# Performance work log

Measured on AMD Instinct MI355X. Metric: run time of the kernel, lower is better.

The kernel has to match this reference:

```python
import jax, jax.numpy as jnp
import numpy as np

N_USERS = 100000
N_ITEMS = 100000
N_EDGES = 200000
TBL = 50            # stored neighbor table width
D = 128             # node feature / embedding dim
TD = 128            # time encoding dim
E = D + TD          # attention embed dim (query = node||time)
H = 2               # heads
DH = E // H
NB = (20, 20)       # n_neighbors per layer
B = 2048
TMAX = 100000


def setup_inputs() -> dict:
    key = jax.random.key(0)
    ks = jax.random.split(key, 32)
    f32 = jnp.float32
    def nrm(k, sh, s):
        return jax.random.normal(k, sh, f32) * s
    inp = {}
    inp["nodes"] = jax.random.randint(ks[0], (B,), 0, N_USERS)
    inp["edges"] = jax.random.randint(ks[1], (B,), 0, N_EDGES)
    inp["timestamps"] = jax.random.randint(ks[2], (B,), 0, TMAX)
    inp["n_layers"] = 2
    # precomputed temporal neighbor tables (buffers) -- user neighbors are items & vice versa
    inp["user_neig"] = jax.random.randint(ks[3], (N_EDGES, TBL), 0, N_ITEMS)
    inp["user_edges"] = jax.random.randint(ks[4], (N_EDGES, TBL), 0, N_EDGES)
    inp["user_times"] = jax.random.randint(ks[5], (N_EDGES, TBL), 0, TMAX)
    inp["user_mask"] = jax.random.randint(ks[6], (N_EDGES, TBL), 0, 2)
    inp["item_neig"] = jax.random.randint(ks[7], (N_EDGES, TBL), 0, N_USERS)
    inp["item_edges"] = jax.random.randint(ks[8], (N_EDGES, TBL), 0, N_EDGES)
    inp["item_times"] = jax.random.randint(ks[9], (N_EDGES, TBL), 0, TMAX)
    inp["item_mask"] = jax.random.randint(ks[10], (N_EDGES, TBL), 0, 2)
    # learned params
    inp["user_emb"] = nrm(ks[11], (N_USERS, D), 0.1)
    inp["item_emb"] = nrm(ks[12], (N_ITEMS, D), 0.1)
    inp["time_w"] = jnp.asarray(1.0 / 10 ** np.linspace(0, 9, TD), f32)
    inp["time_b"] = jnp.zeros((TD,), f32)
    s = 1.0 / np.sqrt(E)
    L = 2
    inp["Wq"] = nrm(ks[13], (L, E, E), s); inp["bq"] = jnp.zeros((L, E), f32)
    inp["Wk"] = nrm(ks[14], (L, E, E), s); inp["bk"] = jnp.zeros((L, E), f32)
    inp["Wv"] = nrm(ks[15], (L, E, E), s); inp["bv"] = jnp.zeros((L, E), f32)
    inp["Wo"] = nrm(ks[16], (L, E, E), s); inp["bo"] = jnp.zeros((L, E), f32)
    inp["W1"] = nrm(ks[17], (L, D, E + D), 1.0 / np.sqrt(E + D)); inp["b1"] = jnp.zeros((L, D), f32)
    inp["W2"] = nrm(ks[18], (L, D, D), 1.0 / np.sqrt(D)); inp["b2"] = jnp.zeros((L, D), f32)
    return inp


def reference(nodes, edges, timestamps, n_layers,
              user_neig, user_edges, user_times, user_mask,
              item_neig, item_edges, item_times, item_mask,
              user_emb, item_emb, time_w, time_b,
              Wq, bq, Wk, bk, Wv, bv, Wo, bo, W1, b1, W2, b2):

    def tenc(t):  # TimeEncode: cos(t * w + b) -> [..., TD]
        return jnp.cos(t.astype(jnp.float32)[..., None] * time_w + time_b)

    def attend(l, node_feat, node_time, nbr_feat, edge_time, mask):
        # query: [N, E]; keys/values: [N, K, E]
        q = jnp.concatenate([node_feat, node_time], axis=-1)
        kv = jnp.concatenate([nbr_feat, edge_time], axis=-1)
        n, k = kv.shape[0], kv.shape[1]
        qh = (q @ Wq[l].T + bq[l]).reshape(n, H, DH)
        kh = (kv @ Wk[l].T + bk[l]).reshape(n, k, H, DH)
        vh = (kv @ Wv[l].T + bv[l]).reshape(n, k, H, DH)
        sc = jnp.einsum('nhd,nkhd->nhk', qh, kh) / np.sqrt(DH)
        valid = mask > 0  # [N, K]
        sc = jnp.where(valid[:, None, :], sc, -1e9)
        a = jax.nn.softmax(sc, axis=-1)
        o = jnp.einsum('nhk,nkhd->nhd', a, vh).reshape(n, E)
        o = o @ Wo[l].T + bo[l]
        o = jnp.where(valid.any(-1, keepdims=True), o, 0.0)  # zero all-invalid rows
        h = jax.nn.relu(jnp.concatenate([o, node_feat], axis=-1) @ W1[l].T + b1[l])
        return h @ W2[l].T + b2[l]

    def compute(nds, eds, tms, layer, is_user):
        nf = (user_emb if is_user else item_emb)[nds]
        if layer == 0:
            return nf
        k = NB[layer - 1]
        if is_user:
            neig, edg, tim, msk = user_neig, user_edges, user_times, user_mask
        else:
            neig, edg, tim, msk = item_neig, item_edges, item_times, item_mask
        adj = neig[eds][:, TBL - k:]   # [N, k] neighbor node ids (opposite type)
        ee = edg[eds][:, TBL - k:]
        tt = tim[eds][:, TBL - k:]
        mm = msk[eds][:, TBL - k:]
        deltas = tms[:, None] - tt
        nbr = compute(adj.reshape(-1), ee.reshape(-1), tt.reshape(-1), layer - 1, not is_user)
        nbr = nbr.reshape(nds.shape[0], k, -1)
        ntime = tenc(jnp.zeros_like(tms))
        etime = tenc(deltas)
        return attend(layer - 1, nf, ntime, nbr, etime, mm)

    return compute(nodes, edges, timestamps, int(n_layers), True)
```

## Files before the change

### kernel.cpp

```cpp
#include <hip/hip_runtime.h>
#include <hip/hip_bf16.h>

#define TBL 50
#define K 20
#define D 128
#define E 256
#define NB_B 2048
#define NSLOT (NB_B*K)
#define G 16

typedef unsigned short ushort;
typedef unsigned short ushort8 __attribute__((ext_vector_type(8)));
typedef float f32x4 __attribute__((ext_vector_type(4)));
typedef __bf16 bf16x8 __attribute__((ext_vector_type(8)));

#define OFF_GC    0
#define OFF_U     1024
#define OFF_CC    1536
#define OFF_PKF   2052
#define OFF_NBRB  264196
#define OFF_CNT   2885636
#define OFF_UEB   2926600
#define WS_NEED_F (OFF_UEB + 6400000)
#define APKo   0
#define VPKo   131072
#define OPKo   262144
#define W1PKo  393216
#define W2PKo  491520

__device__ __forceinline__ float cosr(float x) {
  const float HI = 0.15915493667125702f;
  const float LO = 6.4206383e-9f;
  float k = rintf(x * HI);
  float f = __fmaf_rn(x, HI, -k);
  f = __fmaf_rn(x, LO, f);
  return __builtin_amdgcn_cosf(f);
}
__device__ __forceinline__ float b2f(ushort u) {
  return __uint_as_float(((unsigned)u) << 16);
}
__device__ __forceinline__ ushort cvtbf(float f) {
  unsigned u = __float_as_uint(f);
  return (ushort)((u + 0x7FFF + ((u >> 16) & 1)) >> 16);
}
__device__ __forceinline__ bf16x8 ldb8(const ushort* p) {
  union { ushort8 u; bf16x8 b; } c;
  c.u = *(const ushort8*)p;
  return c.b;
}

__global__ __launch_bounds__(256) void precompute2(
    const float* __restrict__ Wq, const float* __restrict__ Wk,
    const float* __restrict__ bq, const float* __restrict__ bk,
    const float* __restrict__ time_b, float* __restrict__ ws)
{
  __shared__ float sqc[128], ctb[128];
  int b = blockIdx.x, t = threadIdx.x;
  ushort* wsu = (ushort*)(ws + OFF_PKF);
  if (b < 512) {
    int l = b >> 8, h = (b >> 7) & 1, i = b & 127;
    float s = 0.f;
    const float* wq = Wq + l*65536 + h*32768 + i;
    const float* wk = Wk + l*65536 + h*32768 + t;
    for (int m = 0; m < 128; m++) s += wq[m*256]*wk[m*256];
    int N = h*256 + t;
    int nt = N >> 4, cl = N & 15;
    int kk = i >> 5, ch = (i >> 3) & 3, bb = i & 7;
    wsu[APKo + (long)l*65536 + (((nt*4+kk)*64 + ch*16 + cl)*8) + bb] = cvtbf(s);
  } else {
    int q = b - 512, l = q >> 1, h = q & 1;
    if (t < 128) ctb[t] = cosf(time_b[t]);
    __syncthreads();
    if (t < 128) {
      int e = h*128 + t;
      float a = bq[l*256 + e];
      const float* wq = Wq + l*65536 + e*256 + 128;
      for (int m = 0; m < 128; m++) a += wq[m]*ctb[m];
      sqc[t] = a;
    }
    __syncthreads();
    { float s = 0.f;
      const float* wk = Wk + l*65536 + h*32768 + t;
      for (int m = 0; m < 128; m++) s += sqc[m]*wk[m*256];
      ws[OFF_GC + l*512 + h*256 + t] = s; }
    if (t < 128) {
      float s = 0.f;
      const float* wq = Wq + l*65536 + h*32768 + t;
      const float* bkp = bk + l*256 + h*128;
      for (int m = 0; m < 128; m++) s += wq[m*256]*bkp[m];
      ws[OFF_U + (l*2+h)*128 + t] = s; }
    if (t == 254) {
      float s = 0.f;
      const float* bkp = bk + l*256 + h*128;
      for (int m = 0; m < 128; m++) s += sqc[m]*bkp[m];
      ws[OFF_CC + l*2+h] = s; }
  }
}

__global__ __launch_bounds__(256) void packw(
    const float* __restrict__ Wv, const float* __restrict__ Wo,
    const float* __restrict__ W1, const float* __restrict__ W2,
    float* __restrict__ ws)
{
  int idx = blockIdx.x*256 + threadIdx.x;
  ushort* wsu = (ushort*)(ws + OFF_PKF);
  if (idx == 0) *(int*)(ws + OFF_CNT) = 0;
  if (idx < 131072) {
    int q = idx >> 15, r = idx & 32767, l = q >> 1, h = q & 1;
    int bb = r & 7, lane = (r >> 3) & 63, kk = (r >> 9) & 7, nt = r >> 12;
    int k = kk*32 + (lane>>4)*8 + bb, d = nt*16 + (lane&15);
    wsu[VPKo + idx] = cvtbf(Wv[l*65536 + (h*128+d)*256 + k]);
  } else if (idx < 262144) {
    int rel = idx - 131072, l = rel >> 16, r = rel & 65535;
    int bb = r & 7, lane = (r >> 3) & 63, kk = (r >> 9) & 7, nt = r >> 12;
    int k = kk*32 + (lane>>4)*8 + bb, e = nt*16 + (lane&15);
    wsu[OPKo + rel] = cvtbf(Wo[l*65536 + e*256 + k]);
  } else if (idx < 360448) {
    int rel = idx - 262144, l = rel / 49152, r = rel % 49152;
    int nt = r / 6144, rr = r - nt*6144;
    int kk = rr >> 9, lane = (rr >> 3) & 63, bb = rr & 7;
    int k = kk*32 + (lane>>4)*8 + bb, d = nt*16 + (lane&15);
    wsu[W1PKo + rel] = cvtbf(W1[l*49152 + d*384 + k]);
  } else {
    int rel = idx - 360448, l = rel >> 14, r = rel & 16383;
    int nt = r >> 11, rr = r & 2047;
    int kk = rr >> 9, lane = (rr >> 3) & 63, bb = rr & 7;
    int k = kk*32 + (lane>>4)*8 + bb, d = nt*16 + (lane&15);
    wsu[W2PKo + rel] = cvtbf(W2[l*16384 + d*128 + k]);
  }
}

__global__ __launch_bounds__(256) void pack_emb(
    const float* __restrict__ emb, float* __restrict__ ws)
{
  int idx = blockIdx.x*256 + threadIdx.x;
  if (idx < 1600000) {
    float4 a = ((const float4*)emb)[idx*2];
    float4 b = ((const float4*)emb)[idx*2+1];
    ushort8 o;
    o[0]=cvtbf(a.x); o[1]=cvtbf(a.y); o[2]=cvtbf(a.z); o[3]=cvtbf(a.w);
    o[4]=cvtbf(b.x); o[5]=cvtbf(b.y); o[6]=cvtbf(b.z); o[7]=cvtbf(b.w);
    ((ushort8*)(ws + OFF_UEB))[idx] = o;
  }
}

__global__ __launch_bounds__(256) void compact_valid(
    const int* __restrict__ edges, const int* __restrict__ u_mask,
    float* __restrict__ ws)
{
  int idx = blockIdx.x*256 + threadIdx.x;
  int b = idx / K, s = idx - b*K;
  int pe = edges[b];
  if (u_mask[pe*TBL + (TBL-K) + s] > 0) {
    int pos = atomicAdd((int*)(ws + OFF_CNT), 1);
    ((int*)(ws + OFF_CNT))[1 + pos] = idx;
  }
}

template<int LAYER, bool NBF16>
__global__ __launch_bounds__(256, 3) void attend(
    const int* __restrict__ nodes, const int* __restrict__ edges, const int* __restrict__ tstamps,
    const int* __restrict__ u_edges, const int* __restrict__ u_neig,
    const int* __restrict__ u_times, const int* __restrict__ u_mask,
    const int* __restrict__ i_neig, const int* __restrict__ i_times, const int* __restrict__ i_mask,
    const float* __restrict__ user_emb, const float* __restrict__ item_emb,
    const float* __restrict__ time_w, const float* __restrict__ time_b,
    const float* __restrict__ bv, const float* __restrict__ bo,
    const float* __restrict__ b1, const float* __restrict__ b2,
    float* __restrict__ wsf, float* __restrict__ out)
{
  __shared__ __align__(16) ushort sOP2[16*392];
  __shared__ __align__(16) ushort sGWS[16*520];
  __shared__ __align__(16) ushort sOP1[16*264];
  __shared__ float sTW[128], sTB[128], sAL[640], sQB[32];
  __shared__ int imem[96];
  __shared__ int nbm[960];

  const int tid = threadIdx.x, blk = blockIdx.x, l = LAYER;
  const int lane = tid & 63, wv = tid >> 6;
  const int col = lane & 15, chunk = lane >> 4;
  const ushort* wsu = (const ushort*)(wsf + OFF_PKF);
  const ushort* nbu = NBF16 ? ((LAYER == 0) ? (const ushort*)(wsf + OFF_UEB)
                                            : (const ushort*)(wsf + OFF_NBRB))
                            : (const ushort*)nullptr;
  const float*  nbf = user_emb;
  ushort* nbrOut = (ushort*)(wsf + OFF_NBRB);

  int count = (LAYER == 0) ? *(const int*)(wsf + OFF_CNT) : NB_B;
  if (blk*G >= count) return;

  if (tid < G) {
    int idx = blk*G + tid; int act = idx < count ? 1 : 0;
    int slot, nid, ntm, erow;
    if (LAYER == 0) {
      int ii = act ? idx : 0;
      slot = ((const int*)(wsf + OFF_CNT))[1 + ii];
      int bb = slot / K, s = slot - bb*K;
      int base = edges[bb]*TBL + (TBL-K) + s;
      nid = u_neig[base]; ntm = u_times[base]; erow = u_edges[base];
    } else { slot = idx; nid = nodes[idx]; ntm = tstamps[idx]; erow = edges[idx]; }
    imem[tid] = nid; imem[16+tid] = ntm; imem[32+tid] = erow;
    imem[48+tid] = slot; imem[80+tid] = act;
  }
  if (tid < 128) { sTW[tid] = time_w[tid]; sTB[tid] = time_b[tid]; }
  __syncthreads();

  const float* nemb = (LAYER == 0) ? item_emb : user_emb;
  #pragma unroll
  for (int it = 0; it < 8; it++) {
    int idx = tid + it*256, n = idx >> 7, i = idx & 127;
    sOP2[n*392 + 256 + i] = cvtbf(nemb[(long)imem[n]*D + i]);
  }
  #pragma unroll
  for (int it = 0; it < 2; it++) {
    int p = tid + it*256;
    if (p < G*K) {
      int n = p / K, k = p - n*K;
      int base = imem[32+n]*TBL + (TBL-K) + k;
      if (LAYER == 0) { nbm[p] = i_neig[base]; nbm[320+p] = i_times[base]; nbm[640+p] = i_mask[base]; }
      else            { nbm[p] = (blk*G+n)*K + k; nbm[320+p] = u_times[base]; nbm[640+p] = u_mask[base]; }
    }
  }
  __syncthreads();

  {
    bf16x8 a[4];
    #pragma unroll
    for (int kk = 0; kk < 4; kk++)
      a[kk] = ldb8(&sOP2[col*392 + 256 + kk*32 + chunk*8]);
    f32x4 acc[8];
    #pragma unroll
    for (int t = 0; t < 8; t++) acc[t] = (f32x4){0.f,0.f,0.f,0.f};
    const ushort* BP = wsu + APKo + (long)l*65536;
    #pragma unroll
    for (int t = 0; t < 8; t++) {
      int nt = wv*8 + t;
      #pragma unroll
      for (int kk = 0; kk < 4; kk++) {
        bf16x8 b = ldb8(&BP[((nt*4+kk)*64 + lane)*8]);
        acc[t] = __builtin_amdgcn_mfma_f32_16x16x32_bf16(a[kk], b, acc[t], 0, 0, 0);
      }
    }
    #pragma unroll
    for (int t = 0; t < 8; t++) {
      int N = (wv*8+t)*16 + col;
      float gcv = wsf[OFF_GC + l*512 + N];
      #pragma unroll
      for (int r = 0; r < 4; r++)
        sGWS[(chunk*4+r)*520 + N] = cvtbf(acc[t][r] + gcv);
    }
  }
  if (tid < 32) {
    int n = tid >> 1, h = tid & 1;
    float s = wsf[OFF_CC + l*2 + h];
    const float* u = wsf + OFF_U + (l*2+h)*128;
    for (int i = 0; i < 128; i++) s += b2f(sOP2[n*392 + 256 + i])*u[i];
    sQB[tid] = s;
  }
  __syncthreads();

  {
    auto scoreItem = [&](int p) {
      int n = p / K, k = p - n*K;
      float dtf = (float)(imem[16+n] - nbm[320+p]);
      const ushort8* gp = (const ushort8*)&sGWS[n*520];
      float a0 = 0.f, a1 = 0.f;
      if constexpr (NBF16) {
        const ushort8* fr8 = (const ushort8*)(nbu + (long)nbm[p]*D);
        #pragma unroll
        for (int half = 0; half < 2; half++) {
          ushort8 f[8];
          #pragma unroll
          for (int c = 0; c < 8; c++) f[c] = fr8[half*8 + c];
          #pragma unroll
          for (int c = 0; c < 8; c++) {
            ushort8 g0 = gp[half*8 + c], g1 = gp[32 + half*8 + c];
            float f0=b2f(f[c][0]),f1v=b2f(f[c][1]),f2=b2f(f[c][2]),f3=b2f(f[c][3]);
            float f4=b2f(f[c][4]),f5=b2f(f[c][5]),f6=b2f(f[c][6]),f7=b2f(f[c][7]);
            a0 += f0*b2f(g0[0]) + f1v*b2f(g0[1]) + f2*b2f(g0[2]) + f3*b2f(g0[3])
                + f4*b2f(g0[4]) + f5*b2f(g0[5]) + f6*b2f(g0[6]) + f7*b2f(g0[7]);
            a1 += f0*b2f(g1[0]) + f1v*b2f(g1[1]) + f2*b2f(g1[2]) + f3*b2f(g1[3])
                + f4*b2f(g1[4]) + f5*b2f(g1[5]) + f6*b2f(g1[6]) + f7*b2f(g1[7]);
          }
        }
      } else {
        const float4* fr = (const float4*)(nbf + (long)nbm[p]*D);
        #pragma unroll 4
        for (int c = 0; c < 16; c++) {
          float4 f0 = fr[2*c], f1 = fr[2*c+1];
          ushort8 g0 = gp[c], g1 = gp[32+c];
          a0 += f0.x*b2f(g0[0]) + f0.y*b2f(g0[1]) + f0.z*b2f(g0[2]) + f0.w*b2f(g0[3])
              + f1.x*b2f(g0[4]) + f1.y*b2f(g0[5]) + f1.z*b2f(g0[6]) + f1.w*b2f(g0[7]);
          a1 += f0.x*b2f(g1[0]) + f0.y*b2f(g1[1]) + f0.z*b2f(g1[2]) + f0.w*b2f(g1[3])
              + f1.x*b2f(g1[4]) + f1.y*b2f(g1[5]) + f1.z*b2f(g1[6]) + f1.w*b2f(g1[7]);
        }
      }
      #pragma unroll 2
      for (int c = 0; c < 16; c++) {
        ushort8 g0 = gp[16+c], g1 = gp[48+c];
        float a0c = 0.f, a1c = 0.f;
        #pragma unroll
        for (int j = 0; j < 8; j++) {
          float cv = cosr(__fadd_rn(__fmul_rn(dtf, sTW[c*8+j]), sTB[c*8+j]));
          a0c += cv*b2f(g0[j]); a1c += cv*b2f(g1[j]);
        }
        a0 += a0c; a1 += a1c;
      }
      int m = nbm[640+p];
      const float invsq = 0.08838834764831845f;
      sAL[n*40 + k]      = m > 0 ? (a0 + sQB[n*2])*invsq   : -1e9f;
      sAL[n*40 + 20 + k] = m > 0 ? (a1 + sQB[n*2+1])*invsq : -1e9f;
    };
    scoreItem(wv*80 + lane);
    if (lane < 16) scoreItem(wv*80 + 64 + lane);
  }
  __syncthreads();

  if (tid < 2*G) {
    int n = tid >> 1, h = tid & 1;
    float* a = &sAL[n*40 + h*20];
    float mx = -1e30f;
    for (int k = 0; k < K; k++) mx = fmaxf(mx, a[k]);
    float s = 0.f;
    for (int k = 0; k < K; k++) { float e = __expf(a[k]-mx); a[k] = e; s += e; }
    float inv = 1.f/s;
    for (int k = 0; k < K; k++) a[k] *= inv;
    if (h == 0) { int any = 0;
      for (int k = 0; k < K; k++) any |= nbm[640 + n*20 + k];
      imem[64+n] = any; }
  }
  __syncthreads();

  {
    const int n = tid >> 4, e0 = tid & 15;
    float w0[8], w1[8];
    #pragma unroll
    for (int i = 0; i < 8; i++) { w0[i] = 0.f; w1[i] = 0.f; }
    #pragma unroll 4
    for (int k = 0; k < K; k++) {
      float a0k = sAL[n*40 + k], a1k = sAL[n*40 + 20 + k];
      if constexpr (NBF16) {
        ushort8 f = *(const ushort8*)(nbu + (long)nbm[n*20+k]*D + e0*8);
        #pragma unroll
        for (int i = 0; i < 8; i++) {
          float fi = b2f(f[i]);
          w0[i] += a0k*fi; w1[i] += a1k*fi;
        }
      } else {
        const float* fr = nbf + (long)nbm[n*20+k]*D + e0*8;
        float4 fa = *(const float4*)fr, fb = *(const float4*)(fr+4);
        w0[0]+=a0k*fa.x; w1[0]+=a1k*fa.x; w0[1]+=a0k*fa.y; w1[1]+=a1k*fa.y;
        w0[2]+=a0k*fa.z; w1[2]+=a1k*fa.z; w0[3]+=a0k*fa.w; w1[3]+=a1k*fa.w;
        w0[4]+=a0k*fb.x; w1[4]+=a1k*fb.x; w0[5]+=a0k*fb.y; w1[5]+=a1k*fb.y;
        w0[6]+=a0k*fb.z; w1[6]+=a1k*fb.z; w0[7]+=a0k*fb.w; w1[7]+=a1k*fb.w;
      }
    }
    #pragma unroll
    for (int i = 0; i < 8; i++) {
      sGWS[n*520 + e0*8 + i]       = cvtbf(w0[i]);
      sGWS[n*520 + 256 + e0*8 + i] = cvtbf(w1[i]);
    }
    #pragma unroll
    for (int i = 0; i < 8; i++) { w0[i] = 0.f; w1[i] = 0.f; }
    float twv[8], tbv[8];
    #pragma unroll
    for (int i = 0; i < 8; i++) { twv[i] = sTW[e0*8+i]; tbv[i] = sTB[e0*8+i]; }
    for (int k = 0; k < K; k++) {
      float a0k = sAL[n*40 + k], a1k = sAL[n*40 + 20 + k];
      float dtf = (float)(imem[16+n] - nbm[320 + n*20 + k]);
      #pragma unroll
      for (int i = 0; i < 8; i++) {
        float c = cosr(__fadd_rn(__fmul_rn(dtf, twv[i]), tbv[i]));
        w0[i] += a0k*c; w1[i] += a1k*c;
      }
    }
    #pragma unroll
    for (int i = 0; i < 8; i++) {
      sGWS[n*520 + 128 + e0*8 + i] = cvtbf(w0[i]);
      sGWS[n*520 + 384 + e0*8 + i] = cvtbf(w1[i]);
    }
  }
  __syncthreads();

  {
    int h = wv >> 1, ntb = (wv & 1)*4;
    bf16x8 a[8];
    #pragma unroll
    for (int kk = 0; kk < 8; kk++)
      a[kk] = ldb8(&sGWS[col*520 + h*256 + kk*32 + chunk*8]);
    f32x4 acc[4];
    #pragma unroll
    for (int t = 0; t < 4; t++) acc[t] = (f32x4){0.f,0.f,0.f,0.f};
    const ushort* BP = wsu + VPKo + (long)(l*2+h)*32768;
    #pragma unroll
    for (int t = 0; t < 4; t++) {
      int nt = ntb + t;
      #pragma unroll
      for (int kk = 0; kk < 8; kk++) {
        bf16x8 b = ldb8(&BP[((nt*8+kk)*64 + lane)*8]);
        acc[t] = __builtin_amdgcn_mfma_f32_16x16x32_bf16(a[kk], b, acc[t], 0, 0, 0);
      }
    }
    #pragma unroll
    for (int t = 0; t < 4; t++) {
      int ocol = h*128 + (ntb+t)*16 + col;
      float bb = bv[l*256 + ocol];
      #pragma unroll
      for (int r = 0; r < 4; r++)
        sOP1[(chunk*4+r)*264 + ocol] = cvtbf(acc[t][r] + bb);
    }
  }
  __syncthreads();

  {
    bf16x8 a[8];
    #pragma unroll
    for (int kk = 0; kk < 8; kk++)
      a[kk] = ldb8(&sOP1[col*264 + kk*32 + chunk*8]);
    f32x4 acc[4];
    #pragma unroll
    for (int t = 0; t < 4; t++) acc[t] = (f32x4){0.f,0.f,0.f,0.f};
    const ushort* BP = wsu + OPKo + (long)l*65536;
    #pragma unroll
    for (int t = 0; t < 4; t++) {
      int nt = wv*4 + t;
      #pragma unroll
      for (int kk = 0; kk < 8; kk++) {
        bf16x8 b = ldb8(&BP[((nt*8+kk)*64 + lane)*8]);
        acc[t] = __builtin_amdgcn_mfma_f32_16x16x32_bf16(a[kk], b, acc[t], 0, 0, 0);
      }
    }
    #pragma unroll
    for (int t = 0; t < 4; t++) {
      int e = (wv*4+t)*16 + col;
      float bb = bo[l*256 + e];
      #pragma unroll
      for (int r = 0; r < 4; r++) {
        int row = chunk*4 + r;
        float v = imem[64+row] ? (acc[t][r] + bb) : 0.f;
        sOP2[row*392 + e] = cvtbf(v);
      }
    }
  }
  __syncthreads();

  {
    bf16x8 a[12];
    #pragma unroll
    for (int kk = 0; kk < 12; kk++)
      a[kk] = ldb8(&sOP2[col*392 + kk*32 + chunk*8]);
    f32x4 acc[2];
    acc[0] = (f32x4){0.f,0.f,0.f,0.f}; acc[1] = (f32x4){0.f,0.f,0.f,0.f};
    const ushort* BP = wsu + W1PKo + (long)l*49152;
    #pragma unroll
    for (int t = 0; t < 2; t++) {
      int nt = wv*2 + t;
      #pragma unroll
      for (int kk = 0; kk < 12; kk++) {
        bf16x8 b = ldb8(&BP[((nt*12+kk)*64 + lane)*8]);
        acc[t] = __builtin_amdgcn_mfma_f32_16x16x32_bf16(a[kk], b, acc[t], 0, 0, 0);
      }
    }
    #pragma unroll
    for (int t = 0; t < 2; t++) {
      int dcol = (wv*2+t)*16 + col;
      float bb = b1[l*128 + dcol];
      #pragma unroll
      for (int r = 0; r < 4; r++)
        sOP1[(chunk*4+r)*264 + dcol] = cvtbf(fmaxf(acc[t][r] + bb, 0.f));
    }
  }
  __syncthreads();

  {
    bf16x8 a[4];
    #pragma unroll
    for (int kk = 0; kk < 4; kk++)
      a[kk] = ldb8(&sOP1[col*264 + kk*32 + chunk*8]);
    f32x4 acc[2];
    acc[0] = (f32x4){0.f,0.f,0.f,0.f}; acc[1] = (f32x4){0.f,0.f,0.f,0.f};
    const ushort* BP = wsu + W2PKo + (long)l*16384;
    #pragma unroll
    for (int t = 0; t < 2; t++) {
      int nt = wv*2 + t;
      #pragma unroll
      for (int kk = 0; kk < 4; kk++) {
        bf16x8 b = ldb8(&BP[((nt*4+kk)*64 + lane)*8]);
        acc[t] = __builtin_amdgcn_mfma_f32_16x16x32_bf16(a[kk], b, acc[t], 0, 0, 0);
      }
    }
    #pragma unroll
    for (int t = 0; t < 2; t++) {
      int dcol = (wv*2+t)*16 + col;
      float bb = b2[l*128 + dcol];
      #pragma unroll
      for (int r = 0; r < 4; r++) {
        int row = chunk*4 + r;
        float v = acc[t][r] + bb;
        if (LAYER == 0) { if (imem[80+row]) nbrOut[(long)imem[48+row]*D + dcol] = cvtbf(v); }
        else            out[(long)(blk*G + row)*D + dcol] = v;
      }
    }
  }
}

extern "C" void kernel_launch(void* const* d_in, const int* in_sizes, int n_in,
                              void* d_out, int out_size, void* d_ws, size_t ws_size,
                              hipStream_t stream) {
  const int* nodes  = (const int*)d_in[0];
  const int* edges  = (const int*)d_in[1];
  const int* tst    = (const int*)d_in[2];
  const int* u_neig = (const int*)d_in[4];
  const int* u_edges= (const int*)d_in[5];
  const int* u_times= (const int*)d_in[6];
  const int* u_mask = (const int*)d_in[7];
  const int* i_neig = (const int*)d_in[8];
  const int* i_times= (const int*)d_in[10];
  const int* i_mask = (const int*)d_in[11];
  const float* user_emb = (const float*)d_in[12];
  const float* item_emb = (const float*)d_in[13];
  const float* time_w = (const float*)d_in[14];
  const float* time_b = (const float*)d_in[15];
  const float* Wq = (const float*)d_in[16]; const float* bq = (const float*)d_in[17];
  const float* Wk = (const float*)d_in[18]; const float* bk = (const float*)d_in[19];
  const float* Wv = (const float*)d_in[20]; const float* bv = (const float*)d_in[21];
  const float* Wo = (const float*)d_in[22]; const float* bo = (const float*)d_in[23];
  const float* W1 = (const float*)d_in[24]; const float* b1 = (const float*)d_in[25];
  const float* W2 = (const float*)d_in[26]; const float* b2 = (const float*)d_in[27];
  float* ws = (float*)d_ws;
  float* out = (float*)d_out;

  bool emb16 = ws_size >= (size_t)WS_NEED_F * 4;

  precompute2<<<dim3(516), dim3(256), 0, stream>>>(Wq, Wk, bq, bk, time_b, ws);
  packw<<<dim3(1536), dim3(256), 0, stream>>>(Wv, Wo, W1, W2, ws);
  if (emb16) pack_emb<<<dim3(6250), dim3(256), 0, stream>>>(user_emb, ws);
  compact_valid<<<dim3(160), dim3(256), 0, stream>>>(edges, u_mask, ws);

  if (emb16)
    attend<0,true><<<dim3(NSLOT/G), dim3(256), 0, stream>>>(
        nodes, edges, tst, u_edges, u_neig, u_times, u_mask,
        i_neig, i_times, i_mask, user_emb, item_emb, time_w, time_b,
        bv, bo, b1, b2, ws, out);
  else
    attend<0,false><<<dim3(NSLOT/G), dim3(256), 0, stream>>>(
        nodes, edges, tst, u_edges, u_neig, u_times, u_mask,
        i_neig, i_times, i_mask, user_emb, item_emb, time_w, time_b,
        bv, bo, b1, b2, ws, out);

  attend<1,true><<<dim3(NB_B/G), dim3(256), 0, stream>>>(
      nodes, edges, tst, u_edges, u_neig, u_times, u_mask,
      i_neig, i_times, i_mask, user_emb, item_emb, time_w, time_b,
      bv, bo, b1, b2, ws, out);
}
```

Before: 165.3 us.

## Switch bf16 storage and MFMA to fp16 with packed half2 score and aggregation math

Changes every packed weight, embedding and intermediate buffer from bf16 to fp16 and uses the f16 MFMA instead of the bf16 one. The score dot products and the attention-weighted aggregation now accumulate with packed __hfma2 in half precision rather than scalar fp32 FMAs. The score work is also rebalanced so all 256 threads take one full item, and the remaining 64 items are split four ways and combined with shuffles. This aims to halve the VALU work in the score and aggregation loops and to balance the lanes. The cost is fp16 overflow and accumulation-precision risk, notably in the half-precision accumulators and in the -1e9 mask values converted to half.

Result: faster. 143.3 us (-13.3%).

```diff
diff --git a/kernel.cpp b/kernel.cpp
--- a/kernel.cpp
+++ b/kernel.cpp
@@ -1,5 +1,6 @@
 #include <hip/hip_runtime.h>
 #include <hip/hip_bf16.h>
+#include <hip/hip_fp16.h>
 
 #define TBL 50
 #define K 20
@@ -12,7 +13,7 @@
 typedef unsigned short ushort;
 typedef unsigned short ushort8 __attribute__((ext_vector_type(8)));
 typedef float f32x4 __attribute__((ext_vector_type(4)));
-typedef __bf16 bf16x8 __attribute__((ext_vector_type(8)));
+typedef _Float16 half8 __attribute__((ext_vector_type(8)));
 
 #define OFF_GC    0
 #define OFF_U     1024
@@ -36,17 +37,16 @@
   f = __fmaf_rn(x, LO, f);
   return __builtin_amdgcn_cosf(f);
 }
-__device__ __forceinline__ float b2f(ushort u) {
-  return __uint_as_float(((unsigned)u) << 16);
-}
-__device__ __forceinline__ ushort cvtbf(float f) {
-  unsigned u = __float_as_uint(f);
-  return (ushort)((u + 0x7FFF + ((u >> 16) & 1)) >> 16);
-}
-__device__ __forceinline__ bf16x8 ldb8(const ushort* p) {
-  union { ushort8 u; bf16x8 b; } c;
+__device__ __forceinline__ ushort cvth(float f) {
+  union { _Float16 h; ushort u; } c; c.h = (_Float16)f; return c.u;
+}
+__device__ __forceinline__ float h2f(ushort u) {
+  union { ushort u; _Float16 h; } c; c.u = u; return (float)c.h;
+}
+__device__ __forceinline__ half8 ldh8(const ushort* p) {
+  union { ushort8 u; half8 h; } c;
   c.u = *(const ushort8*)p;
-  return c.b;
+  return c.h;
 }
 
 __global__ __launch_bounds__(256) void precompute2(
@@ -66,7 +66,7 @@
     int N = h*256 + t;
     int nt = N >> 4, cl = N & 15;
     int kk = i >> 5, ch = (i >> 3) & 3, bb = i & 7;
-    wsu[APKo + (long)l*65536 + (((nt*4+kk)*64 + ch*16 + cl)*8) + bb] = cvtbf(s);
+    wsu[APKo + (long)l*65536 + (((nt*4+kk)*64 + ch*16 + cl)*8) + bb] = cvth(s);
   } else {
     int q = b - 512, l = q >> 1, h = q & 1;
     if (t < 128) ctb[t] = cosf(time_b[t]);
@@ -109,24 +109,24 @@
     int q = idx >> 15, r = idx & 32767, l = q >> 1, h = q & 1;
     int bb = r & 7, lane = (r >> 3) & 63, kk = (r >> 9) & 7, nt = r >> 12;
     int k = kk*32 + (lane>>4)*8 + bb, d = nt*16 + (lane&15);
-    wsu[VPKo + idx] = cvtbf(Wv[l*65536 + (h*128+d)*256 + k]);
+    wsu[VPKo + idx] = cvth(Wv[l*65536 + (h*128+d)*256 + k]);
   } else if (idx < 262144) {
     int rel = idx - 131072, l = rel >> 16, r = rel & 65535;
     int bb = r & 7, lane = (r >> 3) & 63, kk = (r >> 9) & 7, nt = r >> 12;
     int k = kk*32 + (lane>>4)*8 + bb, e = nt*16 + (lane&15);
-    wsu[OPKo + rel] = cvtbf(Wo[l*65536 + e*256 + k]);
+    wsu[OPKo + rel] = cvth(Wo[l*65536 + e*256 + k]);
   } else if (idx < 360448) {
     int rel = idx - 262144, l = rel / 49152, r = rel % 49152;
     int nt = r / 6144, rr = r - nt*6144;
     int kk = rr >> 9, lane = (rr >> 3) & 63, bb = rr & 7;
     int k = kk*32 + (lane>>4)*8 + bb, d = nt*16 + (lane&15);
-    wsu[W1PKo + rel] = cvtbf(W1[l*49152 + d*384 + k]);
+    wsu[W1PKo + rel] = cvth(W1[l*49152 + d*384 + k]);
   } else {
     int rel = idx - 360448, l = rel >> 14, r = rel & 16383;
     int nt = r >> 11, rr = r & 2047;
     int kk = rr >> 9, lane = (rr >> 3) & 63, bb = rr & 7;
     int k = kk*32 + (lane>>4)*8 + bb, d = nt*16 + (lane&15);
-    wsu[W2PKo + rel] = cvtbf(W2[l*16384 + d*128 + k]);
+    wsu[W2PKo + rel] = cvth(W2[l*16384 + d*128 + k]);
   }
 }
 
@@ -138,8 +138,8 @@
     float4 a = ((const float4*)emb)[idx*2];
     float4 b = ((const float4*)emb)[idx*2+1];
     ushort8 o;
-    o[0]=cvtbf(a.x); o[1]=cvtbf(a.y); o[2]=cvtbf(a.z); o[3]=cvtbf(a.w);
-    o[4]=cvtbf(b.x); o[5]=cvtbf(b.y); o[6]=cvtbf(b.z); o[7]=cvtbf(b.w);
+    o[0]=cvth(a.x); o[1]=cvth(a.y); o[2]=cvth(a.z); o[3]=cvth(a.w);
+    o[4]=cvth(b.x); o[5]=cvth(b.y); o[6]=cvth(b.z); o[7]=cvth(b.w);
     ((ushort8*)(ws + OFF_UEB))[idx] = o;
   }
 }
@@ -209,7 +209,7 @@
   #pragma unroll
   for (int it = 0; it < 8; it++) {
     int idx = tid + it*256, n = idx >> 7, i = idx & 127;
-    sOP2[n*392 + 256 + i] = cvtbf(nemb[(long)imem[n]*D + i]);
+    sOP2[n*392 + 256 + i] = cvth(nemb[(long)imem[n]*D + i]);
   }
   #pragma unroll
   for (int it = 0; it < 2; it++) {
@@ -224,10 +224,10 @@
   __syncthreads();
 
   {
-    bf16x8 a[4];
+    half8 a[4];
     #pragma unroll
     for (int kk = 0; kk < 4; kk++)
-      a[kk] = ldb8(&sOP2[col*392 + 256 + kk*32 + chunk*8]);
+      a[kk] = ldh8(&sOP2[col*392 + 256 + kk*32 + chunk*8]);
     f32x4 acc[8];
     #pragma unroll
     for (int t = 0; t < 8; t++) acc[t] = (f32x4){0.f,0.f,0.f,0.f};
@@ -237,8 +237,8 @@
       int nt = wv*8 + t;
       #pragma unroll
       for (int kk = 0; kk < 4; kk++) {
-        bf16x8 b = ldb8(&BP[((nt*4+kk)*64 + lane)*8]);
-        acc[t] = __builtin_amdgcn_mfma_f32_16x16x32_bf16(a[kk], b, acc[t], 0, 0, 0);
+        half8 b = ldh8(&BP[((nt*4+kk)*64 + lane)*8]);
+        acc[t] = __builtin_amdgcn_mfma_f32_16x16x32_f16(a[kk], b, acc[t], 0, 0, 0);
       }
     }
     #pragma unroll
@@ -247,72 +247,94 @@
       float gcv = wsf[OFF_GC + l*512 + N];
       #pragma unroll
       for (int r = 0; r < 4; r++)
-        sGWS[(chunk*4+r)*520 + N] = cvtbf(acc[t][r] + gcv);
+        sGWS[(chunk*4+r)*520 + N] = cvth(acc[t][r] + gcv);
     }
   }
   if (tid < 32) {
     int n = tid >> 1, h = tid & 1;
     float s = wsf[OFF_CC + l*2 + h];
     const float* u = wsf + OFF_U + (l*2+h)*128;
-    for (int i = 0; i < 128; i++) s += b2f(sOP2[n*392 + 256 + i])*u[i];
+    for (int i = 0; i < 128; i++) s += h2f(sOP2[n*392 + 256 + i])*u[i];
     sQB[tid] = s;
   }
   __syncthreads();
 
   {
-    auto scoreItem = [&](int p) {
-      int n = p / K, k = p - n*K;
+    auto scorePart = [&](int p, int c0, int c1, float& r0, float& r1) {
+      int n = p / K;
       float dtf = (float)(imem[16+n] - nbm[320+p]);
-      const ushort8* gp = (const ushort8*)&sGWS[n*520];
-      float a0 = 0.f, a1 = 0.f;
+      const __half2* gp2 = (const __half2*)&sGWS[n*520];
+      __half2 z = __floats2half2_rn(0.f, 0.f);
+      __half2 A0 = z, B0 = z, A1 = z, B1 = z;
       if constexpr (NBF16) {
-        const ushort8* fr8 = (const ushort8*)(nbu + (long)nbm[p]*D);
-        #pragma unroll
-        for (int half = 0; half < 2; half++) {
-          ushort8 f[8];
-          #pragma unroll
-          for (int c = 0; c < 8; c++) f[c] = fr8[half*8 + c];
-          #pragma unroll
-          for (int c = 0; c < 8; c++) {
-            ushort8 g0 = gp[half*8 + c], g1 = gp[32 + half*8 + c];
-            float f0=b2f(f[c][0]),f1v=b2f(f[c][1]),f2=b2f(f[c][2]),f3=b2f(f[c][3]);
-            float f4=b2f(f[c][4]),f5=b2f(f[c][5]),f6=b2f(f[c][6]),f7=b2f(f[c][7]);
-            a0 += f0*b2f(g0[0]) + f1v*b2f(g0[1]) + f2*b2f(g0[2]) + f3*b2f(g0[3])
-                + f4*b2f(g0[4]) + f5*b2f(g0[5]) + f6*b2f(g0[6]) + f7*b2f(g0[7]);
-            a1 += f0*b2f(g1[0]) + f1v*b2f(g1[1]) + f2*b2f(g1[2]) + f3*b2f(g1[3])
-                + f4*b2f(g1[4]) + f5*b2f(g1[5]) + f6*b2f(g1[6]) + f7*b2f(g1[7]);
-          }
+        const __half2* fr2 = (const __half2*)(nbu + (long)nbm[p]*D);
+        for (int c = c0; c < c1; c++) {
+          __half2 f0 = fr2[c*4+0], f1 = fr2[c*4+1];
+          __half2 f2 = fr2[c*4+2], f3 = fr2[c*4+3];
+          A0 = __hfma2(f0, gp2[c*4+0], A0);     B0 = __hfma2(f1, gp2[c*4+1], B0);
+          A0 = __hfma2(f2, gp2[c*4+2], A0);     B0 = __hfma2(f3, gp2[c*4+3], B0);
+          A1 = __hfma2(f0, gp2[128+c*4+0], A1); B1 = __hfma2(f1, gp2[128+c*4+1], B1);
+          A1 = __hfma2(f2, gp2[128+c*4+2], A1); B1 = __hfma2(f3, gp2[128+c*4+3], B1);
         }
       } else {
-        const float4* fr = (const float4*)(nbf + (long)nbm[p]*D);
-        #pragma unroll 4
-        for (int c = 0; c < 16; c++) {
-          float4 f0 = fr[2*c], f1 = fr[2*c+1];
-          ushort8 g0 = gp[c], g1 = gp[32+c];
-          a0 += f0.x*b2f(g0[0]) + f0.y*b2f(g0[1]) + f0.z*b2f(g0[2]) + f0.w*b2f(g0[3])
-              + f1.x*b2f(g0[4]) + f1.y*b2f(g0[5]) + f1.z*b2f(g0[6]) + f1.w*b2f(g0[7]);
-          a1 += f0.x*b2f(g1[0]) + f0.y*b2f(g1[1]) + f0.z*b2f(g1[2]) + f0.w*b2f(g1[3])
-              + f1.x*b2f(g1[4]) + f1.y*b2f(g1[5]) + f1.z*b2f(g1[6]) + f1.w*b2f(g1[7]);
+        const float* fr = nbf + (long)nbm[p]*D;
+        for (int c = c0; c < c1; c++) {
+          __half2 f0 = __floats2half2_rn(fr[c*8+0], fr[c*8+1]);
+          __half2 f1 = __floats2half2_rn(fr[c*8+2], fr[c*8+3]);
+          __half2 f2 = __floats2half2_rn(fr[c*8+4], fr[c*8+5]);
+          __half2 f3 = __floats2half2_rn(fr[c*8+6], fr[c*8+7]);
+          A0 = __hfma2(f0, gp2[c*4+0], A0);     B0 = __hfma2(f1, gp2[c*4+1], B0);
+          A0 = __hfma2(f2, gp2[c*4+2], A0);     B0 = __hfma2(f3, gp2[c*4+3], B0);
+          A1 = __hfma2(f0, gp2[128+c*4+0], A1); B1 = __hfma2(f1, gp2[128+c*4+1], B1);
+          A1 = __hfma2(f2, gp2[128+c*4+2], A1); B1 = __hfma2(f3, gp2[128+c*4+3], B1);
         }
       }
-      #pragma unroll 2
-      for (int c = 0; c < 16; c++) {
-        ushort8 g0 = gp[16+c], g1 = gp[48+c];
-        float a0c = 0.f, a1c = 0.f;
-        #pragma unroll
-        for (int j = 0; j < 8; j++) {
-          float cv = cosr(__fadd_rn(__fmul_rn(dtf, sTW[c*8+j]), sTB[c*8+j]));
-          a0c += cv*b2f(g0[j]); a1c += cv*b2f(g1[j]);
-        }
-        a0 += a0c; a1 += a1c;
-      }
+      for (int c = c0; c < c1; c++) {
+        int j = c*8;
+        __half2 cA = __floats2half2_rn(
+            cosr(__fadd_rn(__fmul_rn(dtf, sTW[j+0]), sTB[j+0])),
+            cosr(__fadd_rn(__fmul_rn(dtf, sTW[j+1]), sTB[j+1])));
+        __half2 cB = __floats2half2_rn(
+            cosr(__fadd_rn(__fmul_rn(dtf, sTW[j+2]), sTB[j+2])),
+            cosr(__fadd_rn(__fmul_rn(dtf, sTW[j+3]), sTB[j+3])));
+        __half2 cC = __floats2half2_rn(
+            cosr(__fadd_rn(__fmul_rn(dtf, sTW[j+4]), sTB[j+4])),
+            cosr(__fadd_rn(__fmul_rn(dtf, sTW[j+5]), sTB[j+5])));
+        __half2 cD = __floats2half2_rn(
+            cosr(__fadd_rn(__fmul_rn(dtf, sTW[j+6]), sTB[j+6])),
+            cosr(__fadd_rn(__fmul_rn(dtf, sTW[j+7]), sTB[j+7])));
+        A0 = __hfma2(cA, gp2[64+c*4+0], A0);     B0 = __hfma2(cB, gp2[64+c*4+1], B0);
+        A0 = __hfma2(cC, gp2[64+c*4+2], A0);     B0 = __hfma2(cD, gp2[64+c*4+3], B0);
+        A1 = __hfma2(cA, gp2[192+c*4+0], A1);    B1 = __hfma2(cB, gp2[192+c*4+1], B1);
+        A1 = __hfma2(cC, gp2[192+c*4+2], A1);    B1 = __hfma2(cD, gp2[192+c*4+3], B1);
+      }
+      __half2 S0 = __hadd2(A0, B0), S1 = __hadd2(A1, B1);
+      r0 = __low2float(S0) + __high2float(S0);
+      r1 = __low2float(S1) + __high2float(S1);
+    };
+    const float invsq = 0.08838834764831845f;
+    {
+      int p = tid;
+      float a0, a1;
+      scorePart(p, 0, 16, a0, a1);
+      int n = p / K, k = p - n*K;
       int m = nbm[640+p];
-      const float invsq = 0.08838834764831845f;
       sAL[n*40 + k]      = m > 0 ? (a0 + sQB[n*2])*invsq   : -1e9f;
       sAL[n*40 + 20 + k] = m > 0 ? (a1 + sQB[n*2+1])*invsq : -1e9f;
-    };
-    scoreItem(wv*80 + lane);
-    if (lane < 16) scoreItem(wv*80 + 64 + lane);
+    }
+    {
+      int p = 256 + (tid >> 2), sub = tid & 3;
+      float a0, a1;
+      scorePart(p, sub*4, sub*4+4, a0, a1);
+      a0 += __shfl_xor(a0, 1); a0 += __shfl_xor(a0, 2);
+      a1 += __shfl_xor(a1, 1); a1 += __shfl_xor(a1, 2);
+      if (sub == 0) {
+        int n = p / K, k = p - n*K;
+        int m = nbm[640+p];
+        sAL[n*40 + k]      = m > 0 ? (a0 + sQB[n*2])*invsq   : -1e9f;
+        sAL[n*40 + 20 + k] = m > 0 ? (a1 + sQB[n*2+1])*invsq : -1e9f;
+      }
+    }
   }
   __syncthreads();
 
@@ -333,61 +355,69 @@
 
   {
     const int n = tid >> 4, e0 = tid & 15;
-    float w0[8], w1[8];
-    #pragma unroll
-    for (int i = 0; i < 8; i++) { w0[i] = 0.f; w1[i] = 0.f; }
+    __half2 z = __floats2half2_rn(0.f, 0.f);
+    __half2 W0[4], W1[4];
+    #pragma unroll
+    for (int i = 0; i < 4; i++) { W0[i] = z; W1[i] = z; }
     #pragma unroll 4
     for (int k = 0; k < K; k++) {
-      float a0k = sAL[n*40 + k], a1k = sAL[n*40 + 20 + k];
+      __half2 a0h = __half2half2(__float2half(sAL[n*40 + k]));
+      __half2 a1h = __half2half2(__float2half(sAL[n*40 + 20 + k]));
       if constexpr (NBF16) {
-        ushort8 f = *(const ushort8*)(nbu + (long)nbm[n*20+k]*D + e0*8);
+        const __half2* f2 = (const __half2*)(nbu + (long)nbm[n*20+k]*D + e0*8);
         #pragma unroll
-        for (int i = 0; i < 8; i++) {
-          float fi = b2f(f[i]);
-          w0[i] += a0k*fi; w1[i] += a1k*fi;
+        for (int i = 0; i < 4; i++) {
+          __half2 f = f2[i];
+          W0[i] = __hfma2(a0h, f, W0[i]);
+          W1[i] = __hfma2(a1h, f, W1[i]);
         }
       } else {
         const float* fr = nbf + (long)nbm[n*20+k]*D + e0*8;
-        float4 fa = *(const float4*)fr, fb = *(const float4*)(fr+4);
-        w0[0]+=a0k*fa.x; w1[0]+=a1k*fa.x; w0[1]+=a0k*fa.y; w1[1]+=a1k*fa.y;
-        w0[2]+=a0k*fa.z; w1[2]+=a1k*fa.z; w0[3]+=a0k*fa.w; w1[3]+=a1k*fa.w;
-        w0[4]+=a0k*fb.x; w1[4]+=a1k*fb.x; w0[5]+=a0k*fb.y; w1[5]+=a1k*fb.y;
-        w0[6]+=a0k*fb.z; w1[6]+=a1k*fb.z; w0[7]+=a0k*fb.w; w1[7]+=a1k*fb.w;
-      }
-    }
-    #pragma unroll
-    for (int i = 0; i < 8; i++) {
-      sGWS[n*520 + e0*8 + i]       = cvtbf(w0[i]);
-      sGWS[n*520 + 256 + e0*8 + i] = cvtbf(w1[i]);
-    }
-    #pragma unroll
-    for (int i = 0; i < 8; i++) { w0[i] = 0.f; w1[i] = 0.f; }
+        #pragma unroll
+        for (int i = 0; i < 4; i++) {
+          __half2 f = __floats2half2_rn(fr[2*i], fr[2*i+1]);
+          W0[i] = __hfma2(a0h, f, W0[i]);
+          W1[i] = __hfma2(a1h, f, W1[i]);
+        }
+      }
+    }
+    #pragma unroll
+    for (int i = 0; i < 4; i++) {
+      *(__half2*)&sGWS[n*520 + e0*8 + 2*i]       = W0[i];
+      *(__half2*)&sGWS[n*520 + 256 + e0*8 + 2*i] = W1[i];
+    }
+    #pragma unroll
+    for (int i = 0; i < 4; i++) { W0[i] = z; W1[i] = z; }
     float twv[8], tbv[8];
     #pragma unroll
     for (int i = 0; i < 8; i++) { twv[i] = sTW[e0*8+i]; tbv[i] = sTB[e0*8+i]; }
     for (int k = 0; k < K; k++) {
-      float a0k = sAL[n*40 + k], a1k = sAL[n*40 + 20 + k];
+      __half2 a0h = __half2half2(__float2half(sAL[n*40 + k]));
+      __half2 a1h = __half2half2(__float2half(sAL[n*40 + 20 + k]));
       float dtf = (float)(imem[16+n] - nbm[320 + n*20 + k]);
       #pragma unroll
-      for (int i = 0; i < 8; i++) {
-        float c = cosr(__fadd_rn(__fmul_rn(dtf, twv[i]), tbv[i]));
-        w0[i] += a0k*c; w1[i] += a1k*c;
-      }
-    }
-    #pragma unroll
-    for (int i = 0; i < 8; i++) {
-      sGWS[n*520 + 128 + e0*8 + i] = cvtbf(w0[i]);
-      sGWS[n*520 + 384 + e0*8 + i] = cvtbf(w1[i]);
+      for (int i = 0; i < 4; i++) {
+        __half2 c2 = __floats2half2_rn(
+            cosr(__fadd_rn(__fmul_rn(dtf, twv[2*i]),   tbv[2*i])),
+            cosr(__fadd_rn(__fmul_rn(dtf, twv[2*i+1]), tbv[2*i+1])));
+        W0[i] = __hfma2(a0h, c2, W0[i]);
+        W1[i] = __hfma2(a1h, c2, W1[i]);
+      }
+    }
+    #pragma unroll
+    for (int i = 0; i < 4; i++) {
+      *(__half2*)&sGWS[n*520 + 128 + e0*8 + 2*i] = W0[i];
+      *(__half2*)&sGWS[n*520 + 384 + e0*8 + 2*i] = W1[i];
     }
   }
   __syncthreads();
 
   {
     int h = wv >> 1, ntb = (wv & 1)*4;
-    bf16x8 a[8];
+    half8 a[8];
     #pragma unroll
     for (int kk = 0; kk < 8; kk++)
-      a[kk] = ldb8(&sGWS[col*520 + h*256 + kk*32 + chunk*8]);
+      a[kk] = ldh8(&sGWS[col*520 + h*256 + kk*32 + chunk*8]);
     f32x4 acc[4];
     #pragma unroll
     for (int t = 0; t < 4; t++) acc[t] = (f32x4){0.f,0.f,0.f,0.f};
@@ -397,8 +427,8 @@
       int nt = ntb + t;
       #pragma unroll
       for (int kk = 0; kk < 8; kk++) {
-        bf16x8 b = ldb8(&BP[((nt*8+kk)*64 + lane)*8]);
-        acc[t] = __builtin_amdgcn_mfma_f32_16x16x32_bf16(a[kk], b, acc[t], 0, 0, 0);
+        half8 b = ldh8(&BP[((nt*8+kk)*64 + lane)*8]);
+        acc[t] = __builtin_amdgcn_mfma_f32_16x16x32_f16(a[kk], b, acc[t], 0, 0, 0);
       }
     }
     #pragma unroll
@@ -407,16 +437,16 @@
       float bb = bv[l*256 + ocol];
       #pragma unroll
       for (int r = 0; r < 4; r++)
-        sOP1[(chunk*4+r)*264 + ocol] = cvtbf(acc[t][r] + bb);
-    }
-  }
-  __syncthreads();
-
-  {
-    bf16x8 a[8];
+        sOP1[(chunk*4+r)*264 + ocol] = cvth(acc[t][r] + bb);
+    }
+  }
+  __syncthreads();
+
+  {
+    half8 a[8];
     #pragma unroll
     for (int kk = 0; kk < 8; kk++)
-      a[kk] = ldb8(&sOP1[col*264 + kk*32 + chunk*8]);
+      a[kk] = ldh8(&sOP1[col*264 + kk*32 + chunk*8]);
     f32x4 acc[4];
     #pragma unroll
     for (int t = 0; t < 4; t++) acc[t] = (f32x4){0.f,0.f,0.f,0.f};
@@ -426,8 +456,8 @@
       int nt = wv*4 + t;
       #pragma unroll
       for (int kk = 0; kk < 8; kk++) {
-        bf16x8 b = ldb8(&BP[((nt*8+kk)*64 + lane)*8]);
-        acc[t] = __builtin_amdgcn_mfma_f32_16x16x32_bf16(a[kk], b, acc[t], 0, 0, 0);
+        half8 b = ldh8(&BP[((nt*8+kk)*64 + lane)*8]);
+        acc[t] = __builtin_amdgcn_mfma_f32_16x16x32_f16(a[kk], b, acc[t], 0, 0, 0);
       }
     }
     #pragma unroll
@@ -438,17 +468,17 @@
       for (int r = 0; r < 4; r++) {
         int row = chunk*4 + r;
         float v = imem[64+row] ? (acc[t][r] + bb) : 0.f;
-        sOP2[row*392 + e] = cvtbf(v);
-      }
-    }
-  }
-  __syncthreads();
-
-  {
-    bf16x8 a[12];
+        sOP2[row*392 + e] = cvth(v);
+      }
+    }
+  }
+  __syncthreads();
+
+  {
+    half8 a[12];
     #pragma unroll
     for (int kk = 0; kk < 12; kk++)
-      a[kk] = ldb8(&sOP2[col*392 + kk*32 + chunk*8]);
+      a[kk] = ldh8(&sOP2[col*392 + kk*32 + chunk*8]);
     f32x4 acc[2];
     acc[0] = (f32x4){0.f,0.f,0.f,0.f}; acc[1] = (f32x4){0.f,0.f,0.f,0.f};
     const ushort* BP = wsu + W1PKo + (long)l*49152;
@@ -457,8 +487,8 @@
       int nt = wv*2 + t;
       #pragma unroll
       for (int kk = 0; kk < 12; kk++) {
-        bf16x8 b = ldb8(&BP[((nt*12+kk)*64 + lane)*8]);
-        acc[t] = __builtin_amdgcn_mfma_f32_16x16x32_bf16(a[kk], b, acc[t], 0, 0, 0);
+        half8 b = ldh8(&BP[((nt*12+kk)*64 + lane)*8]);
+        acc[t] = __builtin_amdgcn_mfma_f32_16x16x32_f16(a[kk], b, acc[t], 0, 0, 0);
       }
     }
     #pragma unroll
@@ -467,16 +497,16 @@
       float bb = b1[l*128 + dcol];
       #pragma unroll
       for (int r = 0; r < 4; r++)
-        sOP1[(chunk*4+r)*264 + dcol] = cvtbf(fmaxf(acc[t][r] + bb, 0.f));
-    }
-  }
-  __syncthreads();
-
-  {
-    bf16x8 a[4];
+        sOP1[(chunk*4+r)*264 + dcol] = cvth(fmaxf(acc[t][r] + bb, 0.f));
+    }
+  }
+  __syncthreads();
+
+  {
+    half8 a[4];
     #pragma unroll
     for (int kk = 0; kk < 4; kk++)
-      a[kk] = ldb8(&sOP1[col*264 + kk*32 + chunk*8]);
+      a[kk] = ldh8(&sOP1[col*264 + kk*32 + chunk*8]);
     f32x4 acc[2];
     acc[0] = (f32x4){0.f,0.f,0.f,0.f}; acc[1] = (f32x4){0.f,0.f,0.f,0.f};
     const ushort* BP = wsu + W2PKo + (long)l*16384;
@@ -485,8 +515,8 @@
       int nt = wv*2 + t;
       #pragma unroll
       for (int kk = 0; kk < 4; kk++) {
-        bf16x8 b = ldb8(&BP[((nt*4+kk)*64 + lane)*8]);
-        acc[t] = __builtin_amdgcn_mfma_f32_16x16x32_bf16(a[kk], b, acc[t], 0, 0, 0);
+        half8 b = ldh8(&BP[((nt*4+kk)*64 + lane)*8]);
+        acc[t] = __builtin_amdgcn_mfma_f32_16x16x32_f16(a[kk], b, acc[t], 0, 0, 0);
       }
     }
     #pragma unroll
@@ -497,7 +527,7 @@
       for (int r = 0; r < 4; r++) {
         int row = chunk*4 + r;
         float v = acc[t][r] + bb;
-        if (LAYER == 0) { if (imem[80+row]) nbrOut[(long)imem[48+row]*D + dcol] = cvtbf(v); }
+        if (LAYER == 0) { if (imem[80+row]) nbrOut[(long)imem[48+row]*D + dcol] = cvth(v); }
         else            out[(long)(blk*G + row)*D + dcol] = v;
       }
     }
```
